# Kernel tuning notes

Hardware: AMD Instinct MI355X
Metric: run time of the kernel (lower is better)

The kernel has to match this reference:

```python
import jax, jax.numpy as jnp
import numpy as np

N_NODES = 200000
N_EDGES = 800000   # even; edges 2k and 2k+1 are mutual reverses
N_GRAPHS = 8000
HIDDEN = 128
ATOM_FDIM = 39
BOND_FDIM = 11


def setup_inputs() -> dict:
    key = jax.random.key(0)
    ks = jax.random.split(key, 10)
    half = N_EDGES // 2
    u = jax.random.randint(ks[0], (half,), 0, N_NODES, dtype=jnp.int32)
    v = jax.random.randint(ks[1], (half,), 0, N_NODES, dtype=jnp.int32)
    # interleave so that edge 2k = (u,v) and edge 2k+1 = (v,u): reverse(e) = e ^ 1
    src = jnp.stack([u, v], axis=1).reshape(-1)
    dst = jnp.stack([v, u], axis=1).reshape(-1)
    graph_ids = jnp.sort(jax.random.randint(ks[2], (N_NODES,), 0, N_GRAPHS, dtype=jnp.int32))
    atom_x = jax.random.normal(ks[3], (N_NODES, ATOM_FDIM), dtype=jnp.float32)
    bond_x = jax.random.normal(ks[4], (N_EDGES, BOND_FDIM), dtype=jnp.float32)
    W_i = jax.random.normal(ks[5], (HIDDEN, ATOM_FDIM + BOND_FDIM), dtype=jnp.float32) * 0.1
    W_h = jax.random.normal(ks[6], (HIDDEN, HIDDEN), dtype=jnp.float32) * 0.05
    W_o = jax.random.normal(ks[7], (HIDDEN, ATOM_FDIM + HIDDEN), dtype=jnp.float32) * 0.1
    b_o = jnp.zeros((HIDDEN,), dtype=jnp.float32)
    return {"atom_x": atom_x, "bond_x": bond_x, "src": src, "dst": dst,
            "graph_ids": graph_ids, "W_i": W_i, "W_h": W_h, "W_o": W_o,
            "b_o": b_o, "depth": 6, "num_graphs": N_GRAPHS}


def reference(atom_x, bond_x, src, dst, graph_ids, W_i, W_h, W_o, b_o, depth, num_graphs):
    n_nodes = atom_x.shape[0]
    n_edges = bond_x.shape[0]
    # edge e's reverse edge is e XOR 1 (edges are stored as (u,v),(v,u) pairs)
    rev = jnp.bitwise_xor(jnp.arange(n_edges, dtype=jnp.int32), 1)

    # msg_input = W_i @ cat(src_atom_features, bond_features)   (no bias)
    feats = jnp.concatenate([atom_x[src], bond_x], axis=1)       # [E, 50]
    msg_input = feats @ W_i.T                                    # [E, H]
    msg = jax.nn.relu(msg_input)

    # loopy BP over the non-backtracking line graph, depth-1 iterations
    for _ in range(depth - 1):
        node_agg = jax.ops.segment_sum(msg, dst, num_segments=n_nodes)  # [N, H]
        # incoming line-graph messages to edge e=(u,v): all edges into u except reverse(e)
        accum_msg = node_agg[src] - msg[rev]                            # [E, H]
        msg = jax.nn.relu(msg_input + accum_msg @ W_h.T)

    # gather: m[v] = sum of msg over edges into v; h = relu(W_o(cat(x, m)) + b_o)
    m = jax.ops.segment_sum(msg, dst, num_segments=n_nodes)             # [N, H]
    h = jax.nn.relu(jnp.concatenate([atom_x, m], axis=1) @ W_o.T + b_o) # [N, H]

    # mean_nodes: per-graph mean of h
    g_sum = jax.ops.segment_sum(h, graph_ids, num_segments=num_graphs)  # [G, H]
    counts = jax.ops.segment_sum(jnp.ones((n_nodes,), dtype=h.dtype), graph_ids,
                                 num_segments=num_graphs)
    g_repr = g_sum / jnp.maximum(counts, 1.0)[:, None]
    return g_repr
```

## Files before the change

kernel.cpp:

```cpp
#include <hip/hip_runtime.h>
#include <stdint.h>
#include <stddef.h>

#define N_NODES  200000
#define N_EDGES  800000
#define N_GRAPHS 8000
#define HID      128
#define ATOM_F   39
#define BOND_F   11
#define FEAT_F   50
#define KC       192
#define NITER    5
#define SCAN_BLOCKS 196

typedef __bf16 bf16;
typedef __bf16 bf16x2 __attribute__((ext_vector_type(2)));
typedef __bf16 bf16x8 __attribute__((ext_vector_type(8)));
typedef float  f32x2  __attribute__((ext_vector_type(2)));
typedef float  f32x4  __attribute__((ext_vector_type(4)));

__device__ __forceinline__ void split2(float v, bf16& hi, bf16& lo) {
    hi = (bf16)v;
    lo = (bf16)(v - (float)hi);
}


__global__ __launch_bounds__(256) void k_count(const int* __restrict__ dst,
                                               int* __restrict__ deg) {
    int e = blockIdx.x * 256 + threadIdx.x;
    if (e < N_EDGES) atomicAdd(&deg[dst[e]], 1);
}

__global__ __launch_bounds__(256) void k_scanA(const int* __restrict__ deg,
                                               int* __restrict__ bsum) {
    __shared__ int s[256];
    int t = threadIdx.x;
    int base = blockIdx.x * 1024 + t * 4;
    int sum = 0;
    #pragma unroll
    for (int i = 0; i < 4; ++i) { int idx = base + i; if (idx < N_NODES) sum += deg[idx]; }
    s[t] = sum; __syncthreads();
    for (int off = 128; off > 0; off >>= 1) {
        if (t < off) s[t] += s[t + off];
        __syncthreads();
    }
    if (t == 0) bsum[blockIdx.x] = s[0];
}

__global__ __launch_bounds__(256) void k_scanB(int* __restrict__ bsum,
                                               int* __restrict__ ptr) {
    __shared__ int s[256];
    int t = threadIdx.x;
    int v = (t < SCAN_BLOCKS) ? bsum[t] : 0;
    s[t] = v; __syncthreads();
    for (int off = 1; off < 256; off <<= 1) {
        int x = (t >= off) ? s[t - off] : 0;
        __syncthreads();
        s[t] += x;
        __syncthreads();
    }
    if (t < SCAN_BLOCKS) bsum[t] = s[t] - v;
    if (t == 255) ptr[N_NODES] = s[255];
}

__global__ __launch_bounds__(256) void k_scanC(const int* __restrict__ deg,
                                               const int* __restrict__ bsum,
                                               int* __restrict__ ptr,
                                               int* __restrict__ cursor) {
    __shared__ int s[256];
    int t = threadIdx.x;
    int base = blockIdx.x * 1024 + t * 4;
    int v[4]; int sum = 0;
    #pragma unroll
    for (int i = 0; i < 4; ++i) { int idx = base + i; v[i] = (idx < N_NODES) ? deg[idx] : 0; sum += v[i]; }
    s[t] = sum; __syncthreads();
    int tot = sum;
    for (int off = 1; off < 256; off <<= 1) {
        int x = (t >= off) ? s[t - off] : 0;
        __syncthreads();
        s[t] += x;
        __syncthreads();
    }
    int pre = s[t] - tot + bsum[blockIdx.x];
    #pragma unroll
    for (int i = 0; i < 4; ++i) {
        int idx = base + i;
        if (idx < N_NODES) { ptr[idx] = pre; cursor[idx] = pre; pre += v[i]; }
    }
}

__global__ __launch_bounds__(256) void k_fill(const int* __restrict__ dst,
                                              int* __restrict__ cursor,
                                              int* __restrict__ edge_list) {
    int e = blockIdx.x * 256 + threadIdx.x;
    if (e < N_EDGES) {
        int p = atomicAdd(&cursor[dst[e]], 1);
        edge_list[p] = e;
    }
}


__global__ __launch_bounds__(256) void k_prep(const float* __restrict__ Wi,
                                              const float* __restrict__ Wh,
                                              const float* __restrict__ Wo,
                                              bf16* __restrict__ wcb_hi, bf16* __restrict__ wcb_lo,
                                              bf16* __restrict__ wob_hi, bf16* __restrict__ wob_lo) {
    int i = blockIdx.x * 256 + threadIdx.x;
    int o = i / KC, k = i % KC;
    float vc = 0.f;
    if (k < FEAT_F)  vc = Wi[o * FEAT_F + k];
    else if (k >= 64) vc = Wh[o * HID + (k - 64)];
    bf16 hi, lo; split2(vc, hi, lo);
    wcb_hi[i] = hi; wcb_lo[i] = lo;
    float vo = 0.f;
    if (k < ATOM_F)  vo = Wo[o * (ATOM_F + HID) + k];
    else if (k >= 64) vo = Wo[o * (ATOM_F + HID) + ATOM_F + (k - 64)];
    split2(vo, hi, lo);
    wob_hi[i] = hi; wob_lo[i] = lo;
}


template<bool FIRST>
__global__ __launch_bounds__(256, 3) void k_iter(const float* __restrict__ atom_x,
                                                 const float* __restrict__ bond_x,
                                                 const int* __restrict__ src,
                                                 const bf16* __restrict__ node_agg,
                                                 const bf16* __restrict__ wcb_hi,
                                                 const bf16* __restrict__ wcb_lo,
                                                 bf16* __restrict__ msg) {
    constexpr int KS = FIRST ? 2 : 6;
    __shared__ __align__(16) bf16 lds_hi[64 * KC];
    __shared__ __align__(16) bf16 lds_lo[64 * KC];
    const int t = threadIdx.x, w = t >> 6, lane = t & 63;
    const int tile0 = blockIdx.x * 64;
    const int l15 = lane & 15;
    const int l16 = lane & 15;
    const int sub = lane >> 4;
    const int khi = sub * 8;

    int my_src = src[tile0 + lane];

    #pragma unroll
    for (int i = 0; i < 16; ++i) {
        int erow = w * 16 + i;
        int e = tile0 + erow;
        int s = __builtin_amdgcn_readlane(my_src, erow);
        float val = 0.f;
        if (lane < ATOM_F)      val = atom_x[(size_t)s * ATOM_F + lane];
        else if (lane < FEAT_F) val = bond_x[(size_t)e * BOND_F + (lane - ATOM_F)];
        bf16 h, l; split2(val, h, l);
        int col = lane ^ ((i & 7) << 3);
        lds_hi[erow * KC + col] = h;
        lds_lo[erow * KC + col] = l;
    }

    if (!FIRST) {
        #pragma unroll
        for (int g = 0; g < 4; ++g) {
            int erow = w * 16 + g * 4 + sub;
            int e = tile0 + erow;
            int s = __shfl(my_src, erow, 64);
            bf16x8 na8 = *(const bf16x8*)&node_agg[(size_t)s * HID + l16 * 8];
            bf16x8 mg8 = *(const bf16x8*)&msg[(size_t)(e ^ 1) * HID + l16 * 8];
            bf16x8 hi8, lo8;
            #pragma unroll
            for (int q = 0; q < 8; ++q) {
                float d = (float)na8[q] - (float)mg8[q];
                bf16 h, l; split2(d, h, l);
                hi8[q] = h; lo8[q] = l;
            }
            int col = (64 + l16 * 8) ^ ((erow & 7) << 3);
            *(bf16x8*)&lds_hi[erow * KC + col] = hi8;
            *(bf16x8*)&lds_lo[erow * KC + col] = lo8;
        }
    }

    bf16x8 bh[2][KS], bl[2][KS];
    #pragma unroll
    for (int oo = 0; oo < 2; ++oo) {
        int brow = (w * 2 + oo) * 16 + l15;
        #pragma unroll
        for (int ks = 0; ks < KS; ++ks) {
            int boff = brow * KC + ks * 32 + khi;
            bh[oo][ks] = *(const bf16x8*)&wcb_hi[boff];
            bl[oo][ks] = *(const bf16x8*)&wcb_lo[boff];
        }
    }
    __syncthreads();

    f32x4 acc[4][2];
    #pragma unroll
    for (int rf = 0; rf < 4; ++rf)
        #pragma unroll
        for (int oo = 0; oo < 2; ++oo)
            acc[rf][oo] = (f32x4){0.f, 0.f, 0.f, 0.f};

    #pragma unroll
    for (int ks = 0; ks < KS; ++ks) {
        #pragma unroll
        for (int rf = 0; rf < 4; ++rf) {
            int arow = rf * 16 + l15;
            int aoff = arow * KC + ((ks * 32 + khi) ^ ((arow & 7) << 3));
            bf16x8 ah = *(const bf16x8*)&lds_hi[aoff];
            bf16x8 al = *(const bf16x8*)&lds_lo[aoff];
            #pragma unroll
            for (int oo = 0; oo < 2; ++oo) {
                acc[rf][oo] = __builtin_amdgcn_mfma_f32_16x16x32_bf16(ah, bh[oo][ks], acc[rf][oo], 0, 0, 0);
                acc[rf][oo] = __builtin_amdgcn_mfma_f32_16x16x32_bf16(ah, bl[oo][ks], acc[rf][oo], 0, 0, 0);
                acc[rf][oo] = __builtin_amdgcn_mfma_f32_16x16x32_bf16(al, bh[oo][ks], acc[rf][oo], 0, 0, 0);
            }
        }
    }

    #pragma unroll
    for (int rf = 0; rf < 4; ++rf) {
        #pragma unroll
        for (int oo = 0; oo < 2; ++oo) {
            int ocol = (w * 2 + oo) * 16 + l15;
            #pragma unroll
            for (int r = 0; r < 4; ++r) {
                size_t erow2 = (size_t)tile0 + rf * 16 + sub * 4 + r;
                msg[erow2 * HID + ocol] = (bf16)fmaxf(acc[rf][oo][r], 0.f);
            }
        }
    }
}


__global__ __launch_bounds__(256) void k_agg(const bf16* __restrict__ msg,
                                             const int* __restrict__ ptr,
                                             const int* __restrict__ edge_list,
                                             bf16* __restrict__ node_agg) {
    int wid = blockIdx.x * 4 + (threadIdx.x >> 6);
    int lane = threadIdx.x & 63;
    int l16 = lane & 15, sub = lane >> 4;
    int s = ptr[wid];
    int e = ptr[wid + 1];
    float a[8] = {0.f, 0.f, 0.f, 0.f, 0.f, 0.f, 0.f, 0.f};
    for (int i = s; i < e; i += 4) {
        int idx = i + sub;
        if (idx < e) {
            int el = edge_list[idx];
            bf16x8 v = *(const bf16x8*)&msg[(size_t)el * HID + l16 * 8];
            #pragma unroll
            for (int q = 0; q < 8; ++q) a[q] += (float)v[q];
        }
    }
    #pragma unroll
    for (int q = 0; q < 8; ++q) {
        a[q] += __shfl_xor(a[q], 16, 64);
        a[q] += __shfl_xor(a[q], 32, 64);
    }
    if (sub == 0) {
        bf16x8 o;
        #pragma unroll
        for (int q = 0; q < 8; ++q) o[q] = (bf16)a[q];
        *(bf16x8*)&node_agg[(size_t)wid * HID + l16 * 8] = o;
    }
}


__global__ __launch_bounds__(256, 3) void k_out(const float* __restrict__ atom_x,
                                                const bf16* __restrict__ node_agg,
                                                const bf16* __restrict__ wob_hi,
                                                const bf16* __restrict__ wob_lo,
                                                const float* __restrict__ b_o,
                                                const int* __restrict__ graph_ids,
                                                float* __restrict__ out) {
    __shared__ __align__(16) bf16 lds_hi[64 * KC];
    __shared__ __align__(16) bf16 lds_lo[64 * KC];
    const int t = threadIdx.x, w = t >> 6, lane = t & 63;
    const int tile0 = blockIdx.x * 64;
    const int l15 = lane & 15;
    const int l16 = lane & 15;
    const int sub = lane >> 4;
    const int khi = sub * 8;

    #pragma unroll
    for (int i = 0; i < 16; ++i) {
        int nrow = w * 16 + i;
        int v = tile0 + nrow;
        float val = (lane < ATOM_F) ? atom_x[(size_t)v * ATOM_F + lane] : 0.f;
        bf16 h, l; split2(val, h, l);
        int col = lane ^ ((i & 7) << 3);
        lds_hi[nrow * KC + col] = h;
        lds_lo[nrow * KC + col] = l;
    }
    #pragma unroll
    for (int g = 0; g < 4; ++g) {
        int nrow = w * 16 + g * 4 + sub;
        int v = tile0 + nrow;
        bf16x8 m8 = *(const bf16x8*)&node_agg[(size_t)v * HID + l16 * 8];
        bf16x8 hi8, lo8;
        #pragma unroll
        for (int q = 0; q < 8; ++q) {
            bf16 h, l; split2((float)m8[q], h, l);
            hi8[q] = h; lo8[q] = l;
        }
        int col = (64 + l16 * 8) ^ ((nrow & 7) << 3);
        *(bf16x8*)&lds_hi[nrow * KC + col] = hi8;
        *(bf16x8*)&lds_lo[nrow * KC + col] = lo8;
    }

    bf16x8 bh[2][6], bl[2][6];
    #pragma unroll
    for (int oo = 0; oo < 2; ++oo) {
        int brow = (w * 2 + oo) * 16 + l15;
        #pragma unroll
        for (int ks = 0; ks < 6; ++ks) {
            int boff = brow * KC + ks * 32 + khi;
            bh[oo][ks] = *(const bf16x8*)&wob_hi[boff];
            bl[oo][ks] = *(const bf16x8*)&wob_lo[boff];
        }
    }
    __syncthreads();

    f32x4 acc[4][2];
    #pragma unroll
    for (int rf = 0; rf < 4; ++rf)
        #pragma unroll
        for (int oo = 0; oo < 2; ++oo)
            acc[rf][oo] = (f32x4){0.f, 0.f, 0.f, 0.f};

    #pragma unroll
    for (int ks = 0; ks < 6; ++ks) {
        #pragma unroll
        for (int rf = 0; rf < 4; ++rf) {
            int arow = rf * 16 + l15;
            int aoff = arow * KC + ((ks * 32 + khi) ^ ((arow & 7) << 3));
            bf16x8 ah = *(const bf16x8*)&lds_hi[aoff];
            bf16x8 al = *(const bf16x8*)&lds_lo[aoff];
            #pragma unroll
            for (int oo = 0; oo < 2; ++oo) {
                acc[rf][oo] = __builtin_amdgcn_mfma_f32_16x16x32_bf16(ah, bh[oo][ks], acc[rf][oo], 0, 0, 0);
                acc[rf][oo] = __builtin_amdgcn_mfma_f32_16x16x32_bf16(ah, bl[oo][ks], acc[rf][oo], 0, 0, 0);
                acc[rf][oo] = __builtin_amdgcn_mfma_f32_16x16x32_bf16(al, bh[oo][ks], acc[rf][oo], 0, 0, 0);
            }
        }
    }

    #pragma unroll
    for (int rf = 0; rf < 4; ++rf) {
        #pragma unroll
        for (int oo = 0; oo < 2; ++oo) {
            int ocol = (w * 2 + oo) * 16 + l15;
            float bo = b_o[ocol];
            #pragma unroll
            for (int r = 0; r < 4; ++r) {
                int nrow2 = tile0 + rf * 16 + sub * 4 + r;
                int gid = graph_ids[nrow2];
                float hv = fmaxf(acc[rf][oo][r] + bo, 0.f);
                atomicAdd(&out[(size_t)gid * HID + ocol], hv);
            }
        }
    }
}


__global__ __launch_bounds__(256) void k_graphmean(const int* __restrict__ graph_ids,
                                                   float* __restrict__ out) {
    int g = blockIdx.x * 4 + (threadIdx.x >> 6);
    int lane = threadIdx.x & 63;
    int lo = 0, hi = N_NODES;
    while (lo < hi) { int m = (lo + hi) >> 1; if (graph_ids[m] < g) lo = m + 1; else hi = m; }
    int s = lo;
    hi = N_NODES;
    while (lo < hi) { int m = (lo + hi) >> 1; if (graph_ids[m] < g + 1) lo = m + 1; else hi = m; }
    int e = lo;
    float inv = (e > s) ? 1.f / (float)(e - s) : 0.f;
    f32x2* p = (f32x2*)&out[(size_t)g * HID + lane * 2];
    f32x2 v = *p;
    v.x *= inv; v.y *= inv;
    *p = v;
}


__global__ __launch_bounds__(256) void k_sentinel(float* __restrict__ out, float val) {
    int i = blockIdx.x * 256 + threadIdx.x;
    if (i < N_GRAPHS * HID) out[i] = val;
}


extern "C" void kernel_launch(void* const* d_in, const int* in_sizes, int n_in,
                              void* d_out, int out_size, void* d_ws, size_t ws_size,
                              hipStream_t stream) {
    const float* atom_x    = (const float*)d_in[0];
    const float* bond_x    = (const float*)d_in[1];
    const int*   src       = (const int*)d_in[2];
    const int*   dst       = (const int*)d_in[3];
    const int*   graph_ids = (const int*)d_in[4];
    const float* W_i       = (const float*)d_in[5];
    const float* W_h       = (const float*)d_in[6];
    const float* W_o       = (const float*)d_in[7];
    const float* b_o       = (const float*)d_in[8];

    char* ws = (char*)d_ws;
    size_t off = 0;
    auto alloc = [&](size_t bytes) -> char* {
        char* p = ws + off;
        off += (bytes + 255) & ~(size_t)255;
        return p;
    };
    bf16* msg       = (bf16*)alloc((size_t)N_EDGES * HID * 2);
    bf16* node_agg  = (bf16*)alloc((size_t)N_NODES * HID * 2);
    int*  deg       = (int*)alloc((size_t)N_NODES * 4);
    int*  ptr       = (int*)alloc((size_t)(N_NODES + 1) * 4);
    int*  cursor    = (int*)alloc((size_t)N_NODES * 4);
    int*  bsum      = (int*)alloc(1024);
    int*  edge_list = (int*)alloc((size_t)N_EDGES * 4);
    bf16* wcb_hi    = (bf16*)alloc(128 * KC * 2);
    bf16* wcb_lo    = (bf16*)alloc(128 * KC * 2);
    bf16* wob_hi    = (bf16*)alloc(128 * KC * 2);
    bf16* wob_lo    = (bf16*)alloc(128 * KC * 2);

    if (off > ws_size) {
        k_sentinel<<<(N_GRAPHS * HID + 255) / 256, 256, 0, stream>>>((float*)d_out,
                                                                     (float)ws_size);
        return;
    }

    hipMemsetAsync(deg, 0, (size_t)N_NODES * 4, stream);
    hipMemsetAsync(d_out, 0, (size_t)N_GRAPHS * HID * 4, stream);

    k_count<<<N_EDGES / 256, 256, 0, stream>>>(dst, deg);
    k_scanA<<<SCAN_BLOCKS, 256, 0, stream>>>(deg, bsum);
    k_scanB<<<1, 256, 0, stream>>>(bsum, ptr);
    k_scanC<<<SCAN_BLOCKS, 256, 0, stream>>>(deg, bsum, ptr, cursor);
    k_fill<<<N_EDGES / 256, 256, 0, stream>>>(dst, cursor, edge_list);
    k_prep<<<(128 * KC) / 256, 256, 0, stream>>>(W_i, W_h, W_o,
                                                 wcb_hi, wcb_lo, wob_hi, wob_lo);

    k_iter<true><<<N_EDGES / 64, 256, 0, stream>>>(atom_x, bond_x, src, node_agg,
                                                   wcb_hi, wcb_lo, msg);
    for (int it = 0; it < NITER; ++it) {
        k_agg<<<N_NODES / 4, 256, 0, stream>>>(msg, ptr, edge_list, node_agg);
        k_iter<false><<<N_EDGES / 64, 256, 0, stream>>>(atom_x, bond_x, src, node_agg,
                                                        wcb_hi, wcb_lo, msg);
    }
    k_agg<<<N_NODES / 4, 256, 0, stream>>>(msg, ptr, edge_list, node_agg);
    k_out<<<N_NODES / 64, 256, 0, stream>>>(atom_x, node_agg, wob_hi, wob_lo, b_o,
                                            graph_ids, (float*)d_out);
    k_graphmean<<<N_GRAPHS / 4, 256, 0, stream>>>(graph_ids, (float*)d_out);
}
```

Baseline: 3.129 ms.

## Drop low-part split for raw input features and stream weights per k-step

Raw atom and bond features are now stored as a single bf16 (hi only), so the k-chunks holding input features skip the al x bh MFMA and the lo LDS buffer shrinks to 128 columns. Bond features move to column 48, and the weight layout shifts to match. Weight fragments are loaded from global memory inside each k-step instead of being preloaded into registers, and the launch_bounds occupancy hint is removed. This cuts MFMA count, LDS footprint and register pressure, but costs extra global/L2 weight loads inside the loop and lowers input-feature precision to plain bf16.

```diff
diff --git a/kernel.cpp b/kernel.cpp
--- a/kernel.cpp
+++ b/kernel.cpp
@@ -108,12 +108,13 @@
     int i = blockIdx.x * 256 + threadIdx.x;
     int o = i / KC, k = i % KC;
     float vc = 0.f;
-    if (k < FEAT_F)  vc = Wi[o * FEAT_F + k];
-    else if (k >= 64) vc = Wh[o * HID + (k - 64)];
+    if (k < ATOM_F)                        vc = Wi[o * FEAT_F + k];
+    else if (k >= 48 && k < 48 + BOND_F)   vc = Wi[o * FEAT_F + ATOM_F + (k - 48)];
+    else if (k >= 64)                      vc = Wh[o * HID + (k - 64)];
     bf16 hi, lo; split2(vc, hi, lo);
     wcb_hi[i] = hi; wcb_lo[i] = lo;
     float vo = 0.f;
-    if (k < ATOM_F)  vo = Wo[o * (ATOM_F + HID) + k];
+    if (k < ATOM_F)   vo = Wo[o * (ATOM_F + HID) + k];
     else if (k >= 64) vo = Wo[o * (ATOM_F + HID) + ATOM_F + (k - 64)];
     split2(vo, hi, lo);
     wob_hi[i] = hi; wob_lo[i] = lo;
@@ -121,20 +122,19 @@
 
 
 template<bool FIRST>
-__global__ __launch_bounds__(256, 3) void k_iter(const float* __restrict__ atom_x,
-                                                 const float* __restrict__ bond_x,
-                                                 const int* __restrict__ src,
-                                                 const bf16* __restrict__ node_agg,
-                                                 const bf16* __restrict__ wcb_hi,
-                                                 const bf16* __restrict__ wcb_lo,
-                                                 bf16* __restrict__ msg) {
+__global__ __launch_bounds__(256) void k_iter(const float* __restrict__ atom_x,
+                                              const float* __restrict__ bond_x,
+                                              const int* __restrict__ src,
+                                              const bf16* __restrict__ node_agg,
+                                              const bf16* __restrict__ wcb_hi,
+                                              const bf16* __restrict__ wcb_lo,
+                                              bf16* __restrict__ msg) {
     constexpr int KS = FIRST ? 2 : 6;
     __shared__ __align__(16) bf16 lds_hi[64 * KC];
-    __shared__ __align__(16) bf16 lds_lo[64 * KC];
+    __shared__ __align__(16) bf16 lds_lo[64 * 128];
     const int t = threadIdx.x, w = t >> 6, lane = t & 63;
     const int tile0 = blockIdx.x * 64;
     const int l15 = lane & 15;
-    const int l16 = lane & 15;
     const int sub = lane >> 4;
     const int khi = sub * 8;
 
@@ -144,14 +144,12 @@
     for (int i = 0; i < 16; ++i) {
         int erow = w * 16 + i;
         int e = tile0 + erow;
-        int s = __builtin_amdgcn_readlane(my_src, erow);
+        int s = __shfl(my_src, erow, 64);
         float val = 0.f;
-        if (lane < ATOM_F)      val = atom_x[(size_t)s * ATOM_F + lane];
-        else if (lane < FEAT_F) val = bond_x[(size_t)e * BOND_F + (lane - ATOM_F)];
-        bf16 h, l; split2(val, h, l);
+        if (lane < ATOM_F)                      val = atom_x[(size_t)s * ATOM_F + lane];
+        else if (lane >= 48 && lane < 48 + BOND_F) val = bond_x[(size_t)e * BOND_F + (lane - 48)];
         int col = lane ^ ((i & 7) << 3);
-        lds_hi[erow * KC + col] = h;
-        lds_lo[erow * KC + col] = l;
+        lds_hi[erow * KC + col] = (bf16)val;
     }
 
     if (!FIRST) {
@@ -160,8 +158,8 @@
             int erow = w * 16 + g * 4 + sub;
             int e = tile0 + erow;
             int s = __shfl(my_src, erow, 64);
-            bf16x8 na8 = *(const bf16x8*)&node_agg[(size_t)s * HID + l16 * 8];
-            bf16x8 mg8 = *(const bf16x8*)&msg[(size_t)(e ^ 1) * HID + l16 * 8];
+            bf16x8 na8 = *(const bf16x8*)&node_agg[(size_t)s * HID + l15 * 8];
+            bf16x8 mg8 = *(const bf16x8*)&msg[(size_t)(e ^ 1) * HID + l15 * 8];
             bf16x8 hi8, lo8;
             #pragma unroll
             for (int q = 0; q < 8; ++q) {
@@ -169,21 +167,9 @@
                 bf16 h, l; split2(d, h, l);
                 hi8[q] = h; lo8[q] = l;
             }
-            int col = (64 + l16 * 8) ^ ((erow & 7) << 3);
-            *(bf16x8*)&lds_hi[erow * KC + col] = hi8;
-            *(bf16x8*)&lds_lo[erow * KC + col] = lo8;
-        }
-    }
-
-    bf16x8 bh[2][KS], bl[2][KS];
-    #pragma unroll
-    for (int oo = 0; oo < 2; ++oo) {
-        int brow = (w * 2 + oo) * 16 + l15;
-        #pragma unroll
-        for (int ks = 0; ks < KS; ++ks) {
-            int boff = brow * KC + ks * 32 + khi;
-            bh[oo][ks] = *(const bf16x8*)&wcb_hi[boff];
-            bl[oo][ks] = *(const bf16x8*)&wcb_lo[boff];
+            int colg = (l15 * 8) ^ ((erow & 7) << 3);
+            *(bf16x8*)&lds_hi[erow * KC + 64 + colg] = hi8;
+            *(bf16x8*)&lds_lo[erow * 128 + colg] = lo8;
         }
     }
     __syncthreads();
@@ -197,17 +183,29 @@
 
     #pragma unroll
     for (int ks = 0; ks < KS; ++ks) {
+        int kc = ks * 32 + khi;
+        bf16x8 bhf[2], blf[2];
+        #pragma unroll
+        for (int oo = 0; oo < 2; ++oo) {
+            int boff = ((w * 2 + oo) * 16 + l15) * KC + kc;
+            bhf[oo] = *(const bf16x8*)&wcb_hi[boff];
+            blf[oo] = *(const bf16x8*)&wcb_lo[boff];
+        }
         #pragma unroll
         for (int rf = 0; rf < 4; ++rf) {
             int arow = rf * 16 + l15;
-            int aoff = arow * KC + ((ks * 32 + khi) ^ ((arow & 7) << 3));
-            bf16x8 ah = *(const bf16x8*)&lds_hi[aoff];
-            bf16x8 al = *(const bf16x8*)&lds_lo[aoff];
+            int sw = (arow & 7) << 3;
+            bf16x8 ah = *(const bf16x8*)&lds_hi[arow * KC + (kc ^ sw)];
             #pragma unroll
             for (int oo = 0; oo < 2; ++oo) {
-                acc[rf][oo] = __builtin_amdgcn_mfma_f32_16x16x32_bf16(ah, bh[oo][ks], acc[rf][oo], 0, 0, 0);
-                acc[rf][oo] = __builtin_amdgcn_mfma_f32_16x16x32_bf16(ah, bl[oo][ks], acc[rf][oo], 0, 0, 0);
-                acc[rf][oo] = __builtin_amdgcn_mfma_f32_16x16x32_bf16(al, bh[oo][ks], acc[rf][oo], 0, 0, 0);
+                acc[rf][oo] = __builtin_amdgcn_mfma_f32_16x16x32_bf16(ah, bhf[oo], acc[rf][oo], 0, 0, 0);
+                acc[rf][oo] = __builtin_amdgcn_mfma_f32_16x16x32_bf16(ah, blf[oo], acc[rf][oo], 0, 0, 0);
+            }
+            if (ks >= 2) {
+                bf16x8 al = *(const bf16x8*)&lds_lo[arow * 128 + ((kc - 64) ^ sw)];
+                #pragma unroll
+                for (int oo = 0; oo < 2; ++oo)
+                    acc[rf][oo] = __builtin_amdgcn_mfma_f32_16x16x32_bf16(al, bhf[oo], acc[rf][oo], 0, 0, 0);
             }
         }
     }
@@ -260,19 +258,18 @@
 }
 
 
-__global__ __launch_bounds__(256, 3) void k_out(const float* __restrict__ atom_x,
-                                                const bf16* __restrict__ node_agg,
-                                                const bf16* __restrict__ wob_hi,
-                                                const bf16* __restrict__ wob_lo,
-                                                const float* __restrict__ b_o,
-                                                const int* __restrict__ graph_ids,
-                                                float* __restrict__ out) {
+__global__ __launch_bounds__(256) void k_out(const float* __restrict__ atom_x,
+                                             const bf16* __restrict__ node_agg,
+                                             const bf16* __restrict__ wob_hi,
+                                             const bf16* __restrict__ wob_lo,
+                                             const float* __restrict__ b_o,
+                                             const int* __restrict__ graph_ids,
+                                             float* __restrict__ out) {
     __shared__ __align__(16) bf16 lds_hi[64 * KC];
-    __shared__ __align__(16) bf16 lds_lo[64 * KC];
+    __shared__ __align__(16) bf16 lds_lo[64 * 128];
     const int t = threadIdx.x, w = t >> 6, lane = t & 63;
     const int tile0 = blockIdx.x * 64;
     const int l15 = lane & 15;
-    const int l16 = lane & 15;
     const int sub = lane >> 4;
     const int khi = sub * 8;
 
@@ -281,37 +278,22 @@
         int nrow = w * 16 + i;
         int v = tile0 + nrow;
         float val = (lane < ATOM_F) ? atom_x[(size_t)v * ATOM_F + lane] : 0.f;
-        bf16 h, l; split2(val, h, l);
-        int col = lane ^ ((i & 7) << 3);
-        lds_hi[nrow * KC + col] = h;
-        lds_lo[nrow * KC + col] = l;
+        lds_hi[nrow * KC + (lane ^ ((i & 7) << 3))] = (bf16)val;
     }
     #pragma unroll
     for (int g = 0; g < 4; ++g) {
         int nrow = w * 16 + g * 4 + sub;
         int v = tile0 + nrow;
-        bf16x8 m8 = *(const bf16x8*)&node_agg[(size_t)v * HID + l16 * 8];
+        bf16x8 m8 = *(const bf16x8*)&node_agg[(size_t)v * HID + l15 * 8];
         bf16x8 hi8, lo8;
         #pragma unroll
         for (int q = 0; q < 8; ++q) {
             bf16 h, l; split2((float)m8[q], h, l);
             hi8[q] = h; lo8[q] = l;
         }
-        int col = (64 + l16 * 8) ^ ((nrow & 7) << 3);
-        *(bf16x8*)&lds_hi[nrow * KC + col] = hi8;
-        *(bf16x8*)&lds_lo[nrow * KC + col] = lo8;
-    }
-
-    bf16x8 bh[2][6], bl[2][6];
-    #pragma unroll
-    for (int oo = 0; oo < 2; ++oo) {
-        int brow = (w * 2 + oo) * 16 + l15;
-        #pragma unroll
-        for (int ks = 0; ks < 6; ++ks) {
-            int boff = brow * KC + ks * 32 + khi;
-            bh[oo][ks] = *(const bf16x8*)&wob_hi[boff];
-            bl[oo][ks] = *(const bf16x8*)&wob_lo[boff];
-        }
+        int colg = (l15 * 8) ^ ((nrow & 7) << 3);
+        *(bf16x8*)&lds_hi[nrow * KC + 64 + colg] = hi8;
+        *(bf16x8*)&lds_lo[nrow * 128 + colg] = lo8;
     }
     __syncthreads();
 
@@ -324,17 +306,29 @@
 
     #pragma unroll
     for (int ks = 0; ks < 6; ++ks) {
+        int kc = ks * 32 + khi;
+        bf16x8 bhf[2], blf[2];
+        #pragma unroll
+        for (int oo = 0; oo < 2; ++oo) {
+            int boff = ((w * 2 + oo) * 16 + l15) * KC + kc;
+            bhf[oo] = *(const bf16x8*)&wob_hi[boff];
+            blf[oo] = *(const bf16x8*)&wob_lo[boff];
+        }
         #pragma unroll
         for (int rf = 0; rf < 4; ++rf) {
             int arow = rf * 16 + l15;
-            int aoff = arow * KC + ((ks * 32 + khi) ^ ((arow & 7) << 3));
-            bf16x8 ah = *(const bf16x8*)&lds_hi[aoff];
-            bf16x8 al = *(const bf16x8*)&lds_lo[aoff];
+            int sw = (arow & 7) << 3;
+            bf16x8 ah = *(const bf16x8*)&lds_hi[arow * KC + (kc ^ sw)];
             #pragma unroll
             for (int oo = 0; oo < 2; ++oo) {
-                acc[rf][oo] = __builtin_amdgcn_mfma_f32_16x16x32_bf16(ah, bh[oo][ks], acc[rf][oo], 0, 0, 0);
-                acc[rf][oo] = __builtin_amdgcn_mfma_f32_16x16x32_bf16(ah, bl[oo][ks], acc[rf][oo], 0, 0, 0);
-                acc[rf][oo] = __builtin_amdgcn_mfma_f32_16x16x32_bf16(al, bh[oo][ks], acc[rf][oo], 0, 0, 0);
+                acc[rf][oo] = __builtin_amdgcn_mfma_f32_16x16x32_bf16(ah, bhf[oo], acc[rf][oo], 0, 0, 0);
+                acc[rf][oo] = __builtin_amdgcn_mfma_f32_16x16x32_bf16(ah, blf[oo], acc[rf][oo], 0, 0, 0);
+            }
+            if (ks >= 2) {
+                bf16x8 al = *(const bf16x8*)&lds_lo[arow * 128 + ((kc - 64) ^ sw)];
+                #pragma unroll
+                for (int oo = 0; oo < 2; ++oo)
+                    acc[rf][oo] = __builtin_amdgcn_mfma_f32_16x16x32_bf16(al, bhf[oo], acc[rf][oo], 0, 0, 0);
             }
         }
     }
```

New measurement: 2.598 ms. 17.0% less time.
